# Performance work log

Hardware: AMD Instinct MI355X
Metric: run time of the kernel (lower is better)

## Reference

```python
import jax, jax.numpy as jnp
import numpy as np

N_NODES = 30000
N_EDGES = 480000
IN_FEATS = 256
N_HEADS = 8
OUT_FEATS = 32
EDGE_FEATS = 64
NUM_ETYPES = 8
NEG_SLOPE = 0.2


def setup_inputs() -> dict:
    key = jax.random.key(0)
    ks = jax.random.split(key, 14)
    s = 0.05
    return {
        "feat": jax.random.normal(ks[0], (N_NODES, IN_FEATS), dtype=jnp.float32),
        "e_feat": jax.random.randint(ks[1], (N_EDGES,), 0, NUM_ETYPES, dtype=jnp.int32),
        "src": jax.random.randint(ks[2], (N_EDGES,), 0, N_NODES, dtype=jnp.int32),
        "dst": jax.random.randint(ks[3], (N_EDGES,), 0, N_NODES, dtype=jnp.int32),
        # learned params (torch nn.Linear stores weight as [out, in])
        "fc_W": jax.random.normal(ks[4], (N_HEADS * OUT_FEATS, IN_FEATS), dtype=jnp.float32) * s,
        "edge_emb": jax.random.normal(ks[5], (NUM_ETYPES, EDGE_FEATS), dtype=jnp.float32) * s,
        "w_r": jnp.ones((NUM_ETYPES, 1), dtype=jnp.float32),  # init constant 1.0
        "W1": jax.random.normal(ks[6], (EDGE_FEATS * 2, EDGE_FEATS), dtype=jnp.float32) * s,
        "b1": jnp.zeros((EDGE_FEATS * 2,), dtype=jnp.float32),
        "W2": jax.random.normal(ks[7], (EDGE_FEATS * N_HEADS, EDGE_FEATS * 2), dtype=jnp.float32) * s,
        "b2": jnp.zeros((EDGE_FEATS * N_HEADS,), dtype=jnp.float32),
        "attn_l": jax.random.normal(ks[8], (1, N_HEADS, OUT_FEATS), dtype=jnp.float32) * s,
        "attn_r": jax.random.normal(ks[9], (1, N_HEADS, OUT_FEATS), dtype=jnp.float32) * s,
        "attn_e": jax.random.normal(ks[10], (1, N_HEADS, EDGE_FEATS), dtype=jnp.float32) * s,
    }


def reference(feat, e_feat, src, dst, fc_W, edge_emb, w_r, W1, b1, W2, b2,
              attn_l, attn_r, attn_e):
    # node projection: [N, H, D]
    feat_src = (feat @ fc_W.T).reshape(N_NODES, N_HEADS, OUT_FEATS)

    # edge-type embedding -> MLP -> [E, H, edge_feats]
    e_emb = edge_emb[e_feat]                                  # [E, EF]
    h = jax.nn.relu(e_emb @ W1.T + b1)                        # [E, 2*EF]
    e_proc = (h @ W2.T + b2).reshape(-1, N_HEADS, EDGE_FEATS)  # [E, H, EF]

    ee = jnp.sum(e_proc * attn_e, axis=-1)                    # [E, H]
    el = jnp.sum(feat_src * attn_l, axis=-1)                  # [N, H]
    er = jnp.sum(feat_src * attn_r, axis=-1)                  # [N, H]

    logits = jax.nn.leaky_relu(el[src] + er[dst] + ee, NEG_SLOPE)
    logits = logits * w_r[e_feat]                             # relation weight, [E,1] bcast

    # edge_softmax: segment softmax over destination nodes
    emax = jax.ops.segment_max(logits, dst, num_segments=N_NODES)  # [N, H]
    ex = jnp.exp(logits - emax[dst])                               # [E, H]
    denom = jax.ops.segment_sum(ex, dst, num_segments=N_NODES)     # [N, H]
    a = ex / denom[dst]                                            # [E, H]

    # weighted scatter-sum aggregation: rst[v] = sum_{e: dst(e)=v} a_e * feat_src[src(e)]
    msg = feat_src[src] * a[..., None]                             # [E, H, D]
    rst = jax.ops.segment_sum(msg, dst, num_segments=N_NODES)      # [N, H, D]

    return rst, a[..., None]
```

## Files before the change

### kernel.cpp

```cpp
#include <hip/hip_runtime.h>
#include <math.h>

#define N_NODES 30000
#define N_EDGES 480000
#define IN_FEATS 256
#define N_HEADS 8
#define OUT_FEATS 32
#define EDGE_FEATS 64
#define NUM_ETYPES 8
#define NEG_SLOPE 0.2f
#define HD 256

typedef __bf16 bf16_t;
typedef bf16_t bf16x8 __attribute__((ext_vector_type(8)));
typedef float f32x4 __attribute__((ext_vector_type(4)));

__device__ __forceinline__ unsigned short f2bf(float f) {
    unsigned u = __float_as_uint(f);
    u += 0x7fffu + ((u >> 16) & 1u);
    return (unsigned short)(u >> 16);
}
__device__ __forceinline__ float bf2f(unsigned short s) {
    return __uint_as_float(((unsigned)s) << 16);
}

__device__ __forceinline__ void gload_lds16(const void* g, void* l) {
    __builtin_amdgcn_global_load_lds(
        (const __attribute__((address_space(1))) unsigned int*)g,
        (__attribute__((address_space(3))) unsigned int*)l, 16, 0, 0);
}

__global__ void cvt_hist(const float* __restrict__ feat, const float* __restrict__ fcW,
                         const int* __restrict__ dst,
                         unsigned short* __restrict__ featb, unsigned short* __restrict__ fcWb,
                         int* __restrict__ counts) {
    const int n1 = N_NODES * IN_FEATS / 4;
    const int n2 = IN_FEATS * HD / 4;
    const int tid0 = blockIdx.x * blockDim.x + threadIdx.x;
    const int stride = gridDim.x * blockDim.x;
    for (int i = tid0; i < n1 + n2; i += stride) {
        float4 v = (i < n1) ? ((const float4*)feat)[i] : ((const float4*)fcW)[i - n1];
        ushort4 o;
        o.x = f2bf(v.x); o.y = f2bf(v.y); o.z = f2bf(v.z); o.w = f2bf(v.w);
        if (i < n1) ((ushort4*)featb)[i] = o;
        else        ((ushort4*)fcWb)[i - n1] = o;
    }
    for (int e = tid0; e < N_EDGES; e += stride)
        atomicAdd(&counts[dst[e]], 1);
}

__global__ __launch_bounds__(1024) void ee_scan(
    const float* __restrict__ edge_emb,
    const float* __restrict__ W1, const float* __restrict__ b1,
    const float* __restrict__ W2, const float* __restrict__ b2,
    const float* __restrict__ attn_e, float* __restrict__ ee_tab,
    const int* __restrict__ counts, int* __restrict__ offsets,
    int* __restrict__ cursor) {
    __shared__ float h1S[1024];
    __shared__ float MS[1024];
    __shared__ int   buf[30720];
    __shared__ int   sums[1024];
    const int t0 = threadIdx.x;

    {
        int t = t0 >> 7, r = t0 & 127;
        const float4* Wv = (const float4*)(W1 + (size_t)r * EDGE_FEATS);
        const float4* Ev = (const float4*)(edge_emb + (size_t)t * EDGE_FEATS);
        float s = b1[r];
        #pragma unroll
        for (int q = 0; q < 16; q++) {
            float4 w = Wv[q], e = Ev[q];
            s += w.x * e.x + w.y * e.y + w.z * e.z + w.w * e.w;
        }
        h1S[t0] = fmaxf(s, 0.f);
    }
    {
        int h = t0 >> 7, k = t0 & 127;
        float s = 0.f;
        #pragma unroll 8
        for (int f = 0; f < EDGE_FEATS; f++)
            s = fmaf(attn_e[h * EDGE_FEATS + f],
                     W2[(size_t)(h * EDGE_FEATS + f) * (2 * EDGE_FEATS) + k], s);
        MS[t0] = s;
    }
    __syncthreads();
    if (t0 < 64) {
        int t = t0 >> 3, h = t0 & 7;
        float s = 0.f;
        for (int f = 0; f < EDGE_FEATS; f++)
            s = fmaf(attn_e[h * EDGE_FEATS + f], b2[h * EDGE_FEATS + f], s);
        for (int k = 0; k < 2 * EDGE_FEATS; k++)
            s = fmaf(MS[h * 128 + k], h1S[t * 128 + k], s);
        ee_tab[t0] = s;
    }

    for (int i = t0; i < 30720; i += 1024)
        buf[i] = (i < N_NODES) ? counts[i] : 0;
    __syncthreads();
    int s = 0;
    #pragma unroll
    for (int i = 0; i < 30; i++) s += buf[t0 * 30 + i];
    sums[t0] = s;
    __syncthreads();
    for (int off = 1; off < 1024; off <<= 1) {
        int v = (t0 >= off) ? sums[t0 - off] : 0;
        __syncthreads();
        sums[t0] += v;
        __syncthreads();
    }
    int run = sums[t0] - s;
    #pragma unroll
    for (int i = 0; i < 30; i++) {
        int c = buf[t0 * 30 + i];
        buf[t0 * 30 + i] = run;
        run += c;
    }
    __syncthreads();
    for (int i = t0; i < N_NODES; i += 1024) {
        int v = buf[i];
        offsets[i] = v; cursor[i] = v;
    }
}

#define GBM 128
#define GBN 128
#define GBK 64
__global__ __launch_bounds__(512) void gemm_bf16(const unsigned short* __restrict__ A,
                                                 const unsigned short* __restrict__ B,
                                                 const float* __restrict__ attn_l,
                                                 const float* __restrict__ attn_r,
                                                 unsigned short* __restrict__ Cb,
                                                 float* __restrict__ el,
                                                 float* __restrict__ er) {
    __shared__ __align__(16) unsigned char As[2][GBM * GBK * 2];
    __shared__ __align__(16) unsigned char Bs[2][GBN * GBK * 2];
    const int lane = threadIdx.x & 63;
    const int wid = threadIdx.x >> 6;
    const int wr = wid >> 2, wc = wid & 3;
    const int row0 = blockIdx.x * GBM;
    const int col0 = blockIdx.y * GBN;

    f32x4 acc[4][2] = {};

    auto STAGE = [&](int b, int k0) {
        #pragma unroll
        for (int i = 0; i < 2; i++) {
            int loff = (wid * 2 + i) * 1024;
            int row = (loff >> 7) + (lane >> 3);
            int c = lane & 7;
            int gr = row0 + row; if (gr > N_NODES - 1) gr = N_NODES - 1;
            int gc = k0 + ((c ^ (row & 7)) << 3);
            gload_lds16(A + (size_t)gr * IN_FEATS + gc, As[b] + loff + lane * 16);
        }
        #pragma unroll
        for (int i = 0; i < 2; i++) {
            int loff = (wid * 2 + i) * 1024;
            int row = (loff >> 7) + (lane >> 3);
            int c = lane & 7;
            int gc = k0 + ((c ^ (row & 7)) << 3);
            gload_lds16(B + (size_t)(col0 + row) * IN_FEATS + gc, Bs[b] + loff + lane * 16);
        }
    };

    STAGE(0, 0);
    __syncthreads();
    int cur = 0;
    #pragma unroll
    for (int kt = 0; kt < IN_FEATS / GBK; kt++) {
        if (kt < IN_FEATS / GBK - 1) STAGE(cur ^ 1, (kt + 1) * GBK);
        #pragma unroll
        for (int kk = 0; kk < 2; kk++) {
            bf16x8 af[4], bfr[2];
            const int g = kk * 4 + (lane >> 4);
            #pragma unroll
            for (int fm = 0; fm < 4; fm++) {
                int row = wr * 64 + fm * 16 + (lane & 15);
                af[fm] = *(const bf16x8*)(As[cur] + row * 128 + ((g ^ (row & 7)) << 4));
            }
            #pragma unroll
            for (int fn = 0; fn < 2; fn++) {
                int row = wc * 32 + fn * 16 + (lane & 15);
                bfr[fn] = *(const bf16x8*)(Bs[cur] + row * 128 + ((g ^ (row & 7)) << 4));
            }
            #pragma unroll
            for (int fm = 0; fm < 4; fm++)
                #pragma unroll
                for (int fn = 0; fn < 2; fn++)
                    acc[fm][fn] = __builtin_amdgcn_mfma_f32_16x16x32_bf16(
                        af[fm], bfr[fn], acc[fm][fn], 0, 0, 0);
        }
        __syncthreads();
        cur ^= 1;
    }
    #pragma unroll
    for (int fm = 0; fm < 4; fm++) {
        #pragma unroll
        for (int r = 0; r < 4; r++) {
            int row = row0 + wr * 64 + fm * 16 + (lane >> 4) * 4 + r;
            if (row < N_NODES) {
                #pragma unroll
                for (int fn = 0; fn < 2; fn++) {
                    int col = col0 + wc * 32 + fn * 16 + (lane & 15);
                    Cb[(size_t)row * HD + col] = f2bf(acc[fm][fn][r]);
                }
            }
        }
    }
    const int h = col0 / 32 + wc;
    const int d0 = lane & 15;
    const float al0 = attn_l[h * 32 + d0],  al1 = attn_l[h * 32 + d0 + 16];
    const float ar0 = attn_r[h * 32 + d0],  ar1 = attn_r[h * 32 + d0 + 16];
    #pragma unroll
    for (int fm = 0; fm < 4; fm++) {
        #pragma unroll
        for (int r = 0; r < 4; r++) {
            float sl = acc[fm][0][r] * al0 + acc[fm][1][r] * al1;
            float sr = acc[fm][0][r] * ar0 + acc[fm][1][r] * ar1;
            #pragma unroll
            for (int m = 1; m <= 8; m <<= 1) {
                sl += __shfl_xor(sl, m);
                sr += __shfl_xor(sr, m);
            }
            int row = row0 + wr * 64 + fm * 16 + (lane >> 4) * 4 + r;
            if (d0 == 0 && row < N_NODES) {
                el[row * 8 + h] = sl;
                er[row * 8 + h] = sr;
            }
        }
    }
}

__global__ void scatter_kernel(const int* __restrict__ dst, const int* __restrict__ src,
                               const int* __restrict__ etype, int* __restrict__ cursor,
                               int2* __restrict__ sorted2) {
    int e = blockIdx.x * blockDim.x + threadIdx.x;
    if (e >= N_EDGES) return;
    int pos = atomicAdd(&cursor[dst[e]], 1);
    sorted2[pos] = make_int2(src[e] * 8 + etype[e], e);
}

__global__ __launch_bounds__(256) void node_fused(
    const int* __restrict__ offsets, const int* __restrict__ counts,
    const int2* __restrict__ sorted2,
    const float* __restrict__ el, const float* __restrict__ er,
    const float* __restrict__ ee_tab, const float* __restrict__ w_r,
    const unsigned short* __restrict__ fsb,
    float* __restrict__ rst, float* __restrict__ aOut) {
    __shared__ float eeS[64];
    __shared__ float wrS[8];
    __shared__ float lgS[4][64][8];
    __shared__ int   sS[4][8];
    if (threadIdx.x < 64) eeS[threadIdx.x] = ee_tab[threadIdx.x];
    if (threadIdx.x < 8)  wrS[threadIdx.x] = w_r[threadIdx.x];
    __syncthreads();
    const int wv = threadIdx.x >> 6, lane = threadIdx.x & 63;
    const int node = blockIdx.x * 4 + wv;
    if (node >= N_NODES) return;
    const int beg = offsets[node], cnt = counts[node];
    const int e_l = lane >> 3, h = lane & 7;
    const float er_v = er[node * 8 + h];
    const int nch = (cnt + 7) >> 3;

    float m = -1e30f;
    for (int ch = 0; ch < nch; ch++) {
        int idx = ch * 8 + e_l;
        float lg = -1e30f;
        if (idx < cnt) {
            int2 p = sorted2[beg + idx];
            int s = p.x >> 3, t = p.x & 7;
            float x = el[s * 8 + h] + er_v + eeS[t * 8 + h];
            x = (x > 0.f) ? x : NEG_SLOPE * x;
            lg = x * wrS[t];
        }
        if (idx < 64) lgS[wv][idx][h] = lg;
        m = fmaxf(m, lg);
    }
    m = fmaxf(m, __shfl_xor(m, 8));
    m = fmaxf(m, __shfl_xor(m, 16));
    m = fmaxf(m, __shfl_xor(m, 32));

    float sum = 0.f;
    for (int ch = 0; ch < nch; ch++) {
        int idx = ch * 8 + e_l;
        if (idx < cnt) {
            float lg;
            if (idx < 64) lg = lgS[wv][idx][h];
            else {
                int2 p = sorted2[beg + idx];
                int s = p.x >> 3, t = p.x & 7;
                float x = el[s * 8 + h] + er_v + eeS[t * 8 + h];
                x = (x > 0.f) ? x : NEG_SLOPE * x;
                lg = x * wrS[t];
            }
            sum += __expf(lg - m);
        }
    }
    sum += __shfl_xor(sum, 8);
    sum += __shfl_xor(sum, 16);
    sum += __shfl_xor(sum, 32);
    const float inv = 1.f / sum;

    float acc0 = 0.f, acc1 = 0.f, acc2 = 0.f, acc3 = 0.f;
    const int hq = lane >> 3;
    for (int ch = 0; ch < nch; ch++) {
        int idx = ch * 8 + e_l;
        float a = 0.f; int s = 0;
        if (idx < cnt) {
            int2 p = sorted2[beg + idx];
            s = p.x >> 3;
            float lg;
            if (idx < 64) lg = lgS[wv][idx][h];
            else {
                int t = p.x & 7;
                float x = el[s * 8 + h] + er_v + eeS[t * 8 + h];
                x = (x > 0.f) ? x : NEG_SLOPE * x;
                lg = x * wrS[t];
            }
            a = __expf(lg - m) * inv;
            aOut[(size_t)p.y * 8 + h] = a;
        }
        lgS[wv][idx & 63][h] = a;
        if (h == 0) sS[wv][e_l] = s;
        int lim = cnt - ch * 8; if (lim > 8) lim = 8;
        for (int j = 0; j < lim; j++) {
            int sj = sS[wv][j];
            float av = lgS[wv][(ch * 8 + j) & 63][hq];
            ushort4 u = *(const ushort4*)(fsb + (size_t)sj * HD + lane * 4);
            acc0 = fmaf(av, bf2f(u.x), acc0);
            acc1 = fmaf(av, bf2f(u.y), acc1);
            acc2 = fmaf(av, bf2f(u.z), acc2);
            acc3 = fmaf(av, bf2f(u.w), acc3);
        }
    }
    *(float4*)(rst + (size_t)node * HD + lane * 4) = make_float4(acc0, acc1, acc2, acc3);
}

extern "C" void kernel_launch(void* const* d_in, const int* in_sizes, int n_in,
                              void* d_out, int out_size, void* d_ws, size_t ws_size,
                              hipStream_t stream) {
    const float* feat     = (const float*)d_in[0];
    const int*   e_feat   = (const int*)  d_in[1];
    const int*   src      = (const int*)  d_in[2];
    const int*   dst      = (const int*)  d_in[3];
    const float* fc_W     = (const float*)d_in[4];
    const float* edge_emb = (const float*)d_in[5];
    const float* w_r      = (const float*)d_in[6];
    const float* W1       = (const float*)d_in[7];
    const float* b1       = (const float*)d_in[8];
    const float* W2       = (const float*)d_in[9];
    const float* b2       = (const float*)d_in[10];
    const float* attn_l   = (const float*)d_in[11];
    const float* attn_r   = (const float*)d_in[12];
    const float* attn_e   = (const float*)d_in[13];

    char* ws = (char*)d_ws;
    unsigned short* featb  = (unsigned short*)(ws + 0);
    unsigned short* fsb    = (unsigned short*)(ws + 15360000);
    float*          el     = (float*)(ws + 30720000);
    float*          er     = (float*)(ws + 31680000);
    unsigned short* fcWb   = (unsigned short*)(ws + 32640000);
    float*          ee_tab = (float*)(ws + 32771072);
    int*            counts = (int*)(ws + 32771328);
    int*            offs   = (int*)(ws + 32891328);
    int*            cursor = (int*)(ws + 33011328);
    int2*           sorted2= (int2*)(ws + 33131328);

    float* rst  = (float*)d_out;
    float* aOut = rst + (size_t)N_NODES * HD;

    hipMemsetAsync(counts, 0, 120000, stream);
    cvt_hist<<<2048, 256, 0, stream>>>(feat, fc_W, dst, featb, fcWb, counts);
    ee_scan<<<1, 1024, 0, stream>>>(edge_emb, W1, b1, W2, b2, attn_e, ee_tab,
                                    counts, offs, cursor);
    scatter_kernel<<<(N_EDGES + 255) / 256, 256, 0, stream>>>(dst, src, e_feat, cursor, sorted2);
    gemm_bf16<<<dim3((N_NODES + GBM - 1) / GBM, HD / GBN), 512, 0, stream>>>(
        featb, fcWb, attn_l, attn_r, fsb, el, er);
    node_fused<<<(N_NODES + 3) / 4, 256, 0, stream>>>(
        offs, counts, sorted2, el, er, ee_tab, w_r, fsb, rst, aOut);
}
```

Before: 248.8 us.

## Fuse feat bf16 conversion into GEMM, widen N tile, parallelize scan

The separate fp32-to-bf16 pass over feat is removed. The GEMM now loads fp32 feat rows directly, converts them in registers and writes them into swizzled LDS, with the loads for the next tile overlapped with the current MFMA work. The GEMM N tile grows to cover all 256 output columns, so each block computes every head and A is read once per row block. The single-block ee_scan kernel is split into a parallel ee_mid step plus a three-kernel multi-block scan (scanA, eefin_scanB, scanC). The trade-offs are more kernel launches, more registers in the GEMM, and fewer GEMM blocks.

```diff
diff --git a/kernel.cpp b/kernel.cpp
--- a/kernel.cpp
+++ b/kernel.cpp
@@ -10,10 +10,12 @@
 #define NUM_ETYPES 8
 #define NEG_SLOPE 0.2f
 #define HD 256
+#define SCB 118
 
 typedef __bf16 bf16_t;
 typedef bf16_t bf16x8 __attribute__((ext_vector_type(8)));
 typedef float f32x4 __attribute__((ext_vector_type(4)));
+typedef unsigned short ushort8_t __attribute__((ext_vector_type(8)));
 
 __device__ __forceinline__ unsigned short f2bf(float f) {
     unsigned u = __float_as_uint(f);
@@ -30,40 +32,25 @@
         (__attribute__((address_space(3))) unsigned int*)l, 16, 0, 0);
 }
 
-__global__ void cvt_hist(const float* __restrict__ feat, const float* __restrict__ fcW,
-                         const int* __restrict__ dst,
-                         unsigned short* __restrict__ featb, unsigned short* __restrict__ fcWb,
-                         int* __restrict__ counts) {
-    const int n1 = N_NODES * IN_FEATS / 4;
-    const int n2 = IN_FEATS * HD / 4;
-    const int tid0 = blockIdx.x * blockDim.x + threadIdx.x;
-    const int stride = gridDim.x * blockDim.x;
-    for (int i = tid0; i < n1 + n2; i += stride) {
-        float4 v = (i < n1) ? ((const float4*)feat)[i] : ((const float4*)fcW)[i - n1];
+__global__ void hist_cvtW(const int* __restrict__ dst, const float* __restrict__ fcW,
+                          int* __restrict__ counts, unsigned short* __restrict__ fcWb) {
+    int i = blockIdx.x * 256 + threadIdx.x;
+    if (i < IN_FEATS * HD / 4) {
+        float4 v = ((const float4*)fcW)[i];
         ushort4 o;
         o.x = f2bf(v.x); o.y = f2bf(v.y); o.z = f2bf(v.z); o.w = f2bf(v.w);
-        if (i < n1) ((ushort4*)featb)[i] = o;
-        else        ((ushort4*)fcWb)[i - n1] = o;
-    }
-    for (int e = tid0; e < N_EDGES; e += stride)
-        atomicAdd(&counts[dst[e]], 1);
-}
-
-__global__ __launch_bounds__(1024) void ee_scan(
-    const float* __restrict__ edge_emb,
-    const float* __restrict__ W1, const float* __restrict__ b1,
-    const float* __restrict__ W2, const float* __restrict__ b2,
-    const float* __restrict__ attn_e, float* __restrict__ ee_tab,
-    const int* __restrict__ counts, int* __restrict__ offsets,
-    int* __restrict__ cursor) {
-    __shared__ float h1S[1024];
-    __shared__ float MS[1024];
-    __shared__ int   buf[30720];
-    __shared__ int   sums[1024];
-    const int t0 = threadIdx.x;
-
-    {
-        int t = t0 >> 7, r = t0 & 127;
+        ((ushort4*)fcWb)[i] = o;
+    }
+    if (i < N_EDGES) atomicAdd(&counts[dst[i]], 1);
+}
+
+__global__ void ee_mid(const float* __restrict__ edge_emb,
+                       const float* __restrict__ W1, const float* __restrict__ b1,
+                       const float* __restrict__ W2, const float* __restrict__ attn_e,
+                       float* __restrict__ h1_ws, float* __restrict__ M_ws) {
+    int i = blockIdx.x * blockDim.x + threadIdx.x;
+    if (i < 1024) {
+        int t = i >> 7, r = i & 127;
         const float4* Wv = (const float4*)(W1 + (size_t)r * EDGE_FEATS);
         const float4* Ev = (const float4*)(edge_emb + (size_t)t * EDGE_FEATS);
         float s = b1[r];
@@ -72,60 +59,94 @@
             float4 w = Wv[q], e = Ev[q];
             s += w.x * e.x + w.y * e.y + w.z * e.z + w.w * e.w;
         }
-        h1S[t0] = fmaxf(s, 0.f);
-    }
-    {
-        int h = t0 >> 7, k = t0 & 127;
+        h1_ws[i] = fmaxf(s, 0.f);
+    } else {
+        int m = i - 1024;
+        int h = m >> 7, k = m & 127;
         float s = 0.f;
         #pragma unroll 8
         for (int f = 0; f < EDGE_FEATS; f++)
             s = fmaf(attn_e[h * EDGE_FEATS + f],
                      W2[(size_t)(h * EDGE_FEATS + f) * (2 * EDGE_FEATS) + k], s);
-        MS[t0] = s;
-    }
+        M_ws[m] = s;
+    }
+}
+
+__global__ __launch_bounds__(256) void scanA(const int* __restrict__ counts,
+                                             int* __restrict__ partials) {
+    __shared__ int red[256];
+    int i = blockIdx.x * 256 + threadIdx.x;
+    red[threadIdx.x] = (i < N_NODES) ? counts[i] : 0;
     __syncthreads();
-    if (t0 < 64) {
-        int t = t0 >> 3, h = t0 & 7;
+    #pragma unroll
+    for (int off = 128; off > 0; off >>= 1) {
+        if (threadIdx.x < off) red[threadIdx.x] += red[threadIdx.x + off];
+        __syncthreads();
+    }
+    if (threadIdx.x == 0) partials[blockIdx.x] = red[0];
+}
+
+__global__ void eefin_scanB(const int* __restrict__ partials, int* __restrict__ base,
+                            const float* __restrict__ h1_ws, const float* __restrict__ M_ws,
+                            const float* __restrict__ attn_e, const float* __restrict__ b2,
+                            float* __restrict__ ee_tab) {
+    __shared__ int ps[128];
+    int t = threadIdx.x;
+    int v = (t < SCB) ? partials[t] : 0;
+    ps[t] = v;
+    __syncthreads();
+    for (int off = 1; off < 128; off <<= 1) {
+        int u = (t >= off) ? ps[t - off] : 0;
+        __syncthreads();
+        ps[t] += u;
+        __syncthreads();
+    }
+    if (t < SCB) base[t] = ps[t] - v;
+    if (t < 64) {
+        int tt = t >> 3, h = t & 7;
         float s = 0.f;
         for (int f = 0; f < EDGE_FEATS; f++)
             s = fmaf(attn_e[h * EDGE_FEATS + f], b2[h * EDGE_FEATS + f], s);
         for (int k = 0; k < 2 * EDGE_FEATS; k++)
-            s = fmaf(MS[h * 128 + k], h1S[t * 128 + k], s);
-        ee_tab[t0] = s;
-    }
-
-    for (int i = t0; i < 30720; i += 1024)
-        buf[i] = (i < N_NODES) ? counts[i] : 0;
+            s = fmaf(M_ws[h * 128 + k], h1_ws[tt * 128 + k], s);
+        ee_tab[t] = s;
+    }
+}
+
+__global__ __launch_bounds__(256) void scanC(const int* __restrict__ counts,
+                                             const int* __restrict__ base,
+                                             int* __restrict__ offsets,
+                                             int* __restrict__ cursor) {
+    __shared__ int s[256];
+    int t = threadIdx.x;
+    int i = blockIdx.x * 256 + t;
+    int v = (i < N_NODES) ? counts[i] : 0;
+    s[t] = v;
     __syncthreads();
-    int s = 0;
-    #pragma unroll
-    for (int i = 0; i < 30; i++) s += buf[t0 * 30 + i];
-    sums[t0] = s;
-    __syncthreads();
-    for (int off = 1; off < 1024; off <<= 1) {
-        int v = (t0 >= off) ? sums[t0 - off] : 0;
-        __syncthreads();
-        sums[t0] += v;
-        __syncthreads();
-    }
-    int run = sums[t0] - s;
-    #pragma unroll
-    for (int i = 0; i < 30; i++) {
-        int c = buf[t0 * 30 + i];
-        buf[t0 * 30 + i] = run;
-        run += c;
-    }
-    __syncthreads();
-    for (int i = t0; i < N_NODES; i += 1024) {
-        int v = buf[i];
-        offsets[i] = v; cursor[i] = v;
-    }
+    for (int off = 1; off < 256; off <<= 1) {
+        int u = (t >= off) ? s[t - off] : 0;
+        __syncthreads();
+        s[t] += u;
+        __syncthreads();
+    }
+    int o = base[blockIdx.x] + s[t] - v;
+    if (i < N_NODES) { offsets[i] = o; cursor[i] = o; }
+}
+
+__global__ void scatter_kernel(const int* __restrict__ dst, const int* __restrict__ src,
+                               const int* __restrict__ etype, int* __restrict__ cursor,
+                               int2* __restrict__ sorted2) {
+    int e = blockIdx.x * blockDim.x + threadIdx.x;
+    if (e >= N_EDGES) return;
+    int pos = atomicAdd(&cursor[dst[e]], 1);
+    sorted2[pos] = make_int2(src[e] * 8 + etype[e], e);
 }
 
 #define GBM 128
-#define GBN 128
+#define GBN 256
 #define GBK 64
-__global__ __launch_bounds__(512) void gemm_bf16(const unsigned short* __restrict__ A,
+#define NKT (IN_FEATS / GBK)
+__global__ __launch_bounds__(512) void gemm_bf16(const float* __restrict__ A,
                                                  const unsigned short* __restrict__ B,
                                                  const float* __restrict__ attn_l,
                                                  const float* __restrict__ attn_r,
@@ -134,43 +155,66 @@
                                                  float* __restrict__ er) {
     __shared__ __align__(16) unsigned char As[2][GBM * GBK * 2];
     __shared__ __align__(16) unsigned char Bs[2][GBN * GBK * 2];
-    const int lane = threadIdx.x & 63;
-    const int wid = threadIdx.x >> 6;
+    const int tid = threadIdx.x;
+    const int lane = tid & 63;
+    const int wid = tid >> 6;
     const int wr = wid >> 2, wc = wid & 3;
     const int row0 = blockIdx.x * GBM;
-    const int col0 = blockIdx.y * GBN;
-
-    f32x4 acc[4][2] = {};
-
-    auto STAGE = [&](int b, int k0) {
-        #pragma unroll
-        for (int i = 0; i < 2; i++) {
-            int loff = (wid * 2 + i) * 1024;
-            int row = (loff >> 7) + (lane >> 3);
-            int c = lane & 7;
-            int gr = row0 + row; if (gr > N_NODES - 1) gr = N_NODES - 1;
-            int gc = k0 + ((c ^ (row & 7)) << 3);
-            gload_lds16(A + (size_t)gr * IN_FEATS + gc, As[b] + loff + lane * 16);
-        }
-        #pragma unroll
-        for (int i = 0; i < 2; i++) {
-            int loff = (wid * 2 + i) * 1024;
-            int row = (loff >> 7) + (lane >> 3);
-            int c = lane & 7;
-            int gc = k0 + ((c ^ (row & 7)) << 3);
-            gload_lds16(B + (size_t)(col0 + row) * IN_FEATS + gc, Bs[b] + loff + lane * 16);
-        }
-    };
-
-    STAGE(0, 0);
+
+    int arow0 = tid >> 3,        ac0 = tid & 7;
+    int arow1 = (512 + tid) >> 3, ac1 = (512 + tid) & 7;
+    float4 av[2][2];
+
+    f32x4 acc[4][4] = {};
+
+    #pragma unroll
+    for (int i = 0; i < 4; i++) {
+        int loff = (wid * 4 + i) * 1024;
+        int row = (loff >> 7) + (lane >> 3);
+        int c = lane & 7;
+        int gc = ((c ^ (row & 7)) << 3);
+        gload_lds16(B + (size_t)row * IN_FEATS + gc, Bs[0] + loff + lane * 16);
+    }
+    {
+        int gr0 = row0 + arow0; if (gr0 > N_NODES - 1) gr0 = N_NODES - 1;
+        int gr1 = row0 + arow1; if (gr1 > N_NODES - 1) gr1 = N_NODES - 1;
+        const float4* p0 = (const float4*)(A + (size_t)gr0 * IN_FEATS + ac0 * 8);
+        const float4* p1 = (const float4*)(A + (size_t)gr1 * IN_FEATS + ac1 * 8);
+        av[0][0] = p0[0]; av[0][1] = p0[1];
+        av[1][0] = p1[0]; av[1][1] = p1[1];
+        ushort8_t u0, u1;
+        u0[0]=f2bf(av[0][0].x); u0[1]=f2bf(av[0][0].y); u0[2]=f2bf(av[0][0].z); u0[3]=f2bf(av[0][0].w);
+        u0[4]=f2bf(av[0][1].x); u0[5]=f2bf(av[0][1].y); u0[6]=f2bf(av[0][1].z); u0[7]=f2bf(av[0][1].w);
+        u1[0]=f2bf(av[1][0].x); u1[1]=f2bf(av[1][0].y); u1[2]=f2bf(av[1][0].z); u1[3]=f2bf(av[1][0].w);
+        u1[4]=f2bf(av[1][1].x); u1[5]=f2bf(av[1][1].y); u1[6]=f2bf(av[1][1].z); u1[7]=f2bf(av[1][1].w);
+        *(ushort8_t*)(As[0] + arow0 * 128 + ((ac0 ^ (arow0 & 7)) << 4)) = u0;
+        *(ushort8_t*)(As[0] + arow1 * 128 + ((ac1 ^ (arow1 & 7)) << 4)) = u1;
+    }
     __syncthreads();
+
     int cur = 0;
     #pragma unroll
-    for (int kt = 0; kt < IN_FEATS / GBK; kt++) {
-        if (kt < IN_FEATS / GBK - 1) STAGE(cur ^ 1, (kt + 1) * GBK);
+    for (int kt = 0; kt < NKT; kt++) {
+        const int k1 = (kt + 1) * GBK;
+        if (kt + 1 < NKT) {
+            #pragma unroll
+            for (int i = 0; i < 4; i++) {
+                int loff = (wid * 4 + i) * 1024;
+                int row = (loff >> 7) + (lane >> 3);
+                int c = lane & 7;
+                int gc = k1 + ((c ^ (row & 7)) << 3);
+                gload_lds16(B + (size_t)row * IN_FEATS + gc, Bs[cur ^ 1] + loff + lane * 16);
+            }
+            int gr0 = row0 + arow0; if (gr0 > N_NODES - 1) gr0 = N_NODES - 1;
+            int gr1 = row0 + arow1; if (gr1 > N_NODES - 1) gr1 = N_NODES - 1;
+            const float4* p0 = (const float4*)(A + (size_t)gr0 * IN_FEATS + k1 + ac0 * 8);
+            const float4* p1 = (const float4*)(A + (size_t)gr1 * IN_FEATS + k1 + ac1 * 8);
+            av[0][0] = p0[0]; av[0][1] = p0[1];
+            av[1][0] = p1[0]; av[1][1] = p1[1];
+        }
         #pragma unroll
         for (int kk = 0; kk < 2; kk++) {
-            bf16x8 af[4], bfr[2];
+            bf16x8 af[4], bfr[4];
             const int g = kk * 4 + (lane >> 4);
             #pragma unroll
             for (int fm = 0; fm < 4; fm++) {
@@ -178,20 +222,30 @@
                 af[fm] = *(const bf16x8*)(As[cur] + row * 128 + ((g ^ (row & 7)) << 4));
             }
             #pragma unroll
-            for (int fn = 0; fn < 2; fn++) {
-                int row = wc * 32 + fn * 16 + (lane & 15);
+            for (int fn = 0; fn < 4; fn++) {
+                int row = wc * 64 + fn * 16 + (lane & 15);
                 bfr[fn] = *(const bf16x8*)(Bs[cur] + row * 128 + ((g ^ (row & 7)) << 4));
             }
             #pragma unroll
             for (int fm = 0; fm < 4; fm++)
                 #pragma unroll
-                for (int fn = 0; fn < 2; fn++)
+                for (int fn = 0; fn < 4; fn++)
                     acc[fm][fn] = __builtin_amdgcn_mfma_f32_16x16x32_bf16(
                         af[fm], bfr[fn], acc[fm][fn], 0, 0, 0);
         }
+        if (kt + 1 < NKT) {
+            ushort8_t u0, u1;
+            u0[0]=f2bf(av[0][0].x); u0[1]=f2bf(av[0][0].y); u0[2]=f2bf(av[0][0].z); u0[3]=f2bf(av[0][0].w);
+            u0[4]=f2bf(av[0][1].x); u0[5]=f2bf(av[0][1].y); u0[6]=f2bf(av[0][1].z); u0[7]=f2bf(av[0][1].w);
+            u1[0]=f2bf(av[1][0].x); u1[1]=f2bf(av[1][0].y); u1[2]=f2bf(av[1][0].z); u1[3]=f2bf(av[1][0].w);
+            u1[4]=f2bf(av[1][1].x); u1[5]=f2bf(av[1][1].y); u1[6]=f2bf(av[1][1].z); u1[7]=f2bf(av[1][1].w);
+            *(ushort8_t*)(As[cur ^ 1] + arow0 * 128 + ((ac0 ^ (arow0 & 7)) << 4)) = u0;
+            *(ushort8_t*)(As[cur ^ 1] + arow1 * 128 + ((ac1 ^ (arow1 & 7)) << 4)) = u1;
+        }
         __syncthreads();
         cur ^= 1;
     }
+
     #pragma unroll
     for (int fm = 0; fm < 4; fm++) {
         #pragma unroll
@@ -199,44 +253,38 @@
             int row = row0 + wr * 64 + fm * 16 + (lane >> 4) * 4 + r;
             if (row < N_NODES) {
                 #pragma unroll
-                for (int fn = 0; fn < 2; fn++) {
-                    int col = col0 + wc * 32 + fn * 16 + (lane & 15);
+                for (int fn = 0; fn < 4; fn++) {
+                    int col = wc * 64 + fn * 16 + (lane & 15);
                     Cb[(size_t)row * HD + col] = f2bf(acc[fm][fn][r]);
                 }
             }
         }
     }
-    const int h = col0 / 32 + wc;
     const int d0 = lane & 15;
-    const float al0 = attn_l[h * 32 + d0],  al1 = attn_l[h * 32 + d0 + 16];
-    const float ar0 = attn_r[h * 32 + d0],  ar1 = attn_r[h * 32 + d0 + 16];
     #pragma unroll
-    for (int fm = 0; fm < 4; fm++) {
+    for (int hp = 0; hp < 2; hp++) {
+        const int h = wc * 2 + hp;
+        const float al0 = attn_l[h * 32 + d0], al1 = attn_l[h * 32 + d0 + 16];
+        const float ar0 = attn_r[h * 32 + d0], ar1 = attn_r[h * 32 + d0 + 16];
         #pragma unroll
-        for (int r = 0; r < 4; r++) {
-            float sl = acc[fm][0][r] * al0 + acc[fm][1][r] * al1;
-            float sr = acc[fm][0][r] * ar0 + acc[fm][1][r] * ar1;
+        for (int fm = 0; fm < 4; fm++) {
             #pragma unroll
-            for (int m = 1; m <= 8; m <<= 1) {
-                sl += __shfl_xor(sl, m);
-                sr += __shfl_xor(sr, m);
-            }
-            int row = row0 + wr * 64 + fm * 16 + (lane >> 4) * 4 + r;
-            if (d0 == 0 && row < N_NODES) {
-                el[row * 8 + h] = sl;
-                er[row * 8 + h] = sr;
-            }
-        }
-    }
-}
-
-__global__ void scatter_kernel(const int* __restrict__ dst, const int* __restrict__ src,
-                               const int* __restrict__ etype, int* __restrict__ cursor,
-                               int2* __restrict__ sorted2) {
-    int e = blockIdx.x * blockDim.x + threadIdx.x;
-    if (e >= N_EDGES) return;
-    int pos = atomicAdd(&cursor[dst[e]], 1);
-    sorted2[pos] = make_int2(src[e] * 8 + etype[e], e);
+            for (int r = 0; r < 4; r++) {
+                float sl = acc[fm][2 * hp][r] * al0 + acc[fm][2 * hp + 1][r] * al1;
+                float sr = acc[fm][2 * hp][r] * ar0 + acc[fm][2 * hp + 1][r] * ar1;
+                #pragma unroll
+                for (int m = 1; m <= 8; m <<= 1) {
+                    sl += __shfl_xor(sl, m);
+                    sr += __shfl_xor(sr, m);
+                }
+                int row = row0 + wr * 64 + fm * 16 + (lane >> 4) * 4 + r;
+                if (d0 == 0 && row < N_NODES) {
+                    el[row * 8 + h] = sl;
+                    er[row * 8 + h] = sr;
+                }
+            }
+        }
+    }
 }
 
 __global__ __launch_bounds__(256) void node_fused(
@@ -354,27 +402,32 @@
     const float* attn_e   = (const float*)d_in[13];
 
     char* ws = (char*)d_ws;
-    unsigned short* featb  = (unsigned short*)(ws + 0);
-    unsigned short* fsb    = (unsigned short*)(ws + 15360000);
-    float*          el     = (float*)(ws + 30720000);
-    float*          er     = (float*)(ws + 31680000);
-    unsigned short* fcWb   = (unsigned short*)(ws + 32640000);
-    float*          ee_tab = (float*)(ws + 32771072);
-    int*            counts = (int*)(ws + 32771328);
-    int*            offs   = (int*)(ws + 32891328);
-    int*            cursor = (int*)(ws + 33011328);
-    int2*           sorted2= (int2*)(ws + 33131328);
+    unsigned short* fsb     = (unsigned short*)(ws + 0);
+    float*          el      = (float*)(ws + 15360000);
+    float*          er      = (float*)(ws + 16320000);
+    unsigned short* fcWb    = (unsigned short*)(ws + 17280000);
+    float*          ee_tab  = (float*)(ws + 17411072);
+    int*            counts  = (int*)(ws + 17411328);
+    int*            offs    = (int*)(ws + 17531328);
+    int*            cursor  = (int*)(ws + 17651328);
+    int2*           sorted2 = (int2*)(ws + 17771328);
+    float*          h1_ws   = (float*)(ws + 21611328);
+    float*          M_ws    = (float*)(ws + 21615424);
+    int*            partials= (int*)(ws + 21619520);
+    int*            base    = (int*)(ws + 21620032);
 
     float* rst  = (float*)d_out;
     float* aOut = rst + (size_t)N_NODES * HD;
 
     hipMemsetAsync(counts, 0, 120000, stream);
-    cvt_hist<<<2048, 256, 0, stream>>>(feat, fc_W, dst, featb, fcWb, counts);
-    ee_scan<<<1, 1024, 0, stream>>>(edge_emb, W1, b1, W2, b2, attn_e, ee_tab,
-                                    counts, offs, cursor);
+    hist_cvtW<<<(N_EDGES + 255) / 256, 256, 0, stream>>>(dst, fc_W, counts, fcWb);
+    ee_mid<<<8, 256, 0, stream>>>(edge_emb, W1, b1, W2, attn_e, h1_ws, M_ws);
+    scanA<<<SCB, 256, 0, stream>>>(counts, partials);
+    eefin_scanB<<<1, 128, 0, stream>>>(partials, base, h1_ws, M_ws, attn_e, b2, ee_tab);
+    scanC<<<SCB, 256, 0, stream>>>(counts, base, offs, cursor);
     scatter_kernel<<<(N_EDGES + 255) / 256, 256, 0, stream>>>(dst, src, e_feat, cursor, sorted2);
-    gemm_bf16<<<dim3((N_NODES + GBM - 1) / GBM, HD / GBN), 512, 0, stream>>>(
-        featb, fcWb, attn_l, attn_r, fsb, el, er);
+    gemm_bf16<<<(N_NODES + GBM - 1) / GBM, 512, 0, stream>>>(
+        feat, fcWb, attn_l, attn_r, fsb, el, er);
     node_fused<<<(N_NODES + 3) / 4, 256, 0, stream>>>(
         offs, counts, sorted2, el, er, ee_tab, w_r, fsb, rst, aOut);
 }
```

New measurement: 229.1 us. -7.9%, faster.
